# Performance work log

Measured on AMD Instinct MI355X. Metric: run time of the kernel, lower is better.

## Reference

```python
import jax, jax.numpy as jnp
import numpy as np

E, D, H, F = 1024, 64, 16, 4096  # embedding, per-head dim, heads, mlp hidden
B, S = 2, 2048
EPS = 1e-5


def _layernorm(x, g, b):
    m = jnp.mean(x, axis=-1, keepdims=True)
    v = jnp.mean((x - m) ** 2, axis=-1, keepdims=True)
    return (x - m) * jax.lax.rsqrt(v + EPS) * g + b


def setup_inputs() -> dict:
    key = jax.random.key(0)
    ks = jax.random.split(key, 12)
    s_e = 1.0 / np.sqrt(E)
    s_f = 1.0 / np.sqrt(F)
    return {
        "x": jax.random.normal(ks[0], (B, S, E), jnp.float32),
        "Wq": jax.random.normal(ks[1], (H, E, D), jnp.float32) * s_e,
        "bq": jnp.zeros((H, D), jnp.float32),
        "Wk": jax.random.normal(ks[2], (H, E, D), jnp.float32) * s_e,
        "bk": jnp.zeros((H, D), jnp.float32),
        "Wv": jax.random.normal(ks[3], (H, E, D), jnp.float32) * s_e,
        "bv": jnp.zeros((H, D), jnp.float32),
        "Wo": jax.random.normal(ks[4], (E, E), jnp.float32) * s_e,
        "bo": jnp.zeros((E,), jnp.float32),
        "ln1_g": jnp.ones((E,), jnp.float32),
        "ln1_b": jnp.zeros((E,), jnp.float32),
        "ln2_g": jnp.ones((E,), jnp.float32),
        "ln2_b": jnp.zeros((E,), jnp.float32),
        "W1": jax.random.normal(ks[5], (E, F), jnp.float32) * s_e,
        "b1": jnp.zeros((F,), jnp.float32),
        "W2": jax.random.normal(ks[6], (F, E), jnp.float32) * s_f,
        "b2": jnp.zeros((E,), jnp.float32),
    }


def reference(x, Wq, bq, Wk, bk, Wv, bv, Wo, bo, ln1_g, ln1_b, ln2_g, ln2_b, W1, b1, W2, b2):
    h = _layernorm(x, ln1_g, ln1_b)
    # batched-head projections: [H,B,S,D]
    q = jnp.einsum("bse,hed->hbsd", h, Wq) + bq[:, None, None, :]
    k = jnp.einsum("bse,hed->hbsd", h, Wk) + bk[:, None, None, :]
    v = jnp.einsum("bse,hed->hbsd", h, Wv) + bv[:, None, None, :]
    # faithful quirk: scores = K @ Q^T (no 1/sqrt(d)), softmax over query axis
    scores = jnp.einsum("hbsd,hbtd->hbst", k, q)  # [H,B,S_key,S_query]
    att = jax.nn.softmax(scores, axis=-1)
    o = jnp.einsum("hbst,hbtd->hbsd", att, v)  # [H,B,S,D]
    o = jnp.transpose(o, (1, 2, 0, 3)).reshape(x.shape[0], x.shape[1], -1)  # concat heads
    x = x + o @ Wo + bo
    m = _layernorm(x, ln2_g, ln2_b)
    m = jax.nn.relu(m @ W1 + b1) @ W2 + b2
    return x + m
```

## Files before the change

### kernel.cpp

```cpp
#include <hip/hip_runtime.h>
#include <cstdint>
#include <cstddef>

typedef __attribute__((ext_vector_type(8))) short short8;
typedef __attribute__((ext_vector_type(4))) float f32x4;
typedef __attribute__((ext_vector_type(4))) unsigned short ushort4v;

#define E_DIM 1024
#define D_DIM 64
#define H_DIM 16
#define F_DIM 4096
#define B_DIM 2
#define S_DIM 2048
#define M_DIM 4096
#define LN_EPS 1e-5f

__device__ __forceinline__ float bf2f(unsigned short u) {
  union { unsigned int i; float f; } v;
  v.i = ((unsigned int)u) << 16;
  return v.f;
}
__device__ __forceinline__ unsigned short f2bf(float f) {
  union { float f; unsigned int i; } v;
  v.f = f;
  unsigned int r = v.i + 0x7FFFu + ((v.i >> 16) & 1u);
  return (unsigned short)(r >> 16);
}

__device__ __forceinline__ void gload_lds16(const unsigned short* src,
                                            unsigned short* dst) {
  __builtin_amdgcn_global_load_lds(
      (const __attribute__((address_space(1))) void*)src,
      (__attribute__((address_space(3))) void*)dst, 16, 0, 0);
}

template <bool QKV>
__global__ __launch_bounds__(256) void transpose_w(
    const float* __restrict__ in, unsigned short* __restrict__ ohi, int R,
    int C) {
  __shared__ float t[32][33];
  const int c0 = blockIdx.x * 32, r0 = blockIdx.y * 32;
  const int tid = threadIdx.x;
  {
    const int rr = tid >> 3, c4 = (tid & 7) * 4;
    size_t addr;
    if (QKV)
      addr = (size_t)(c0 >> 6) * 65536 + (size_t)(r0 + rr) * 64 +
             ((c0 & 63) + c4);
    else
      addr = (size_t)(r0 + rr) * C + (c0 + c4);
    float4 v = *(const float4*)(in + addr);
    t[rr][c4 + 0] = v.x;
    t[rr][c4 + 1] = v.y;
    t[rr][c4 + 2] = v.z;
    t[rr][c4 + 3] = v.w;
  }
  __syncthreads();
  {
    const int cc = tid >> 3, k4 = (tid & 7) * 4;
    ushort4v hi;
    hi.x = f2bf(t[k4 + 0][cc]);
    hi.y = f2bf(t[k4 + 1][cc]);
    hi.z = f2bf(t[k4 + 2][cc]);
    hi.w = f2bf(t[k4 + 3][cc]);
    *(ushort4v*)(ohi + (size_t)(c0 + cc) * R + (r0 + k4)) = hi;
  }
}

__global__ __launch_bounds__(256) void ln_kernel(const float* __restrict__ x,
                                                 const float* __restrict__ g,
                                                 const float* __restrict__ b,
                                                 unsigned short* __restrict__ o) {
  const int row = blockIdx.x;
  const float* xp = x + (size_t)row * E_DIM;
  const int t4 = threadIdx.x * 4;
  float4 xv = *(const float4*)(xp + t4);
  float s = xv.x + xv.y + xv.z + xv.w;
  float ss = xv.x * xv.x + xv.y * xv.y + xv.z * xv.z + xv.w * xv.w;
#pragma unroll
  for (int off = 32; off > 0; off >>= 1) {
    s += __shfl_down(s, off);
    ss += __shfl_down(ss, off);
  }
  __shared__ float red[8];
  const int wid = threadIdx.x >> 6;
  if ((threadIdx.x & 63) == 0) {
    red[wid] = s;
    red[4 + wid] = ss;
  }
  __syncthreads();
  if (threadIdx.x == 0) {
    float S = red[0] + red[1] + red[2] + red[3];
    float SS = red[4] + red[5] + red[6] + red[7];
    float mean = S * (1.0f / E_DIM);
    float var = SS * (1.0f / E_DIM) - mean * mean;
    red[0] = mean;
    red[1] = rsqrtf(var + LN_EPS);
  }
  __syncthreads();
  const float mean = red[0], rstd = red[1];
  float4 gv = *(const float4*)(g + t4);
  float4 bv = *(const float4*)(b + t4);
  ushort4v hi;
  hi.x = f2bf((xv.x - mean) * rstd * gv.x + bv.x);
  hi.y = f2bf((xv.y - mean) * rstd * gv.y + bv.y);
  hi.z = f2bf((xv.z - mean) * rstd * gv.z + bv.z);
  hi.w = f2bf((xv.w - mean) * rstd * gv.w + bv.w);
  *(ushort4v*)(o + (size_t)row * E_DIM + t4) = hi;
}

template <int MODE>
__global__ __launch_bounds__(256) void mfma_gemm(
    const unsigned short* __restrict__ A, const unsigned short* __restrict__ B,
    const float* __restrict__ bias, const float* __restrict__ bias2,
    const float* __restrict__ bias3, const float* __restrict__ resid,
    void* __restrict__ out0, void* __restrict__ out1, void* __restrict__ out2,
    int M, int N, int K) {
  __shared__ unsigned short As[8192];
  __shared__ unsigned short Bs[8192];
  const int tid = threadIdx.x;
  const int m0 = blockIdx.y * 128, n0 = blockIdx.x * 128;
  const int lane = tid & 63, wid = tid >> 6;
  const int wr = wid >> 1, wc = wid & 1;
  const int lr = lane & 15, lg = lane >> 4;

  f32x4 acc[4][4];
#pragma unroll
  for (int i = 0; i < 4; ++i)
#pragma unroll
    for (int j = 0; j < 4; ++j) acc[i][j] = {0.f, 0.f, 0.f, 0.f};

  const int kbeg = (MODE == 4) ? blockIdx.z * 1024 : 0;
  const int kend = (MODE == 4) ? kbeg + 1024 : K;

  for (int k0 = kbeg; k0 < kend; k0 += 64) {
#pragma unroll
    for (int c = 0; c < 4; ++c) {
      int slot = tid + 256 * c;
      int r = slot >> 3;
      int cb = ((slot & 7) << 4) ^ ((r & 7) << 4);
      int ldsoff = tid * 8 + c * 2048;
      gload_lds16(A + (size_t)(m0 + r) * K + k0 + (cb >> 1), As + ldsoff);
      gload_lds16(B + (size_t)(n0 + r) * K + k0 + (cb >> 1), Bs + ldsoff);
    }
    __syncthreads();
#pragma unroll
    for (int kc = 0; kc < 2; ++kc) {
      short8 af[4], bf[4];
#pragma unroll
      for (int mi = 0; mi < 4; ++mi) {
        int r = wr * 64 + mi * 16 + lr;
        int cb = (kc * 64 + lg * 16) ^ ((r & 7) << 4);
        af[mi] = *(const short8*)(As + r * 64 + (cb >> 1));
      }
#pragma unroll
      for (int ni = 0; ni < 4; ++ni) {
        int r = wc * 64 + ni * 16 + lr;
        int cb = (kc * 64 + lg * 16) ^ ((r & 7) << 4);
        bf[ni] = *(const short8*)(Bs + r * 64 + (cb >> 1));
      }
#pragma unroll
      for (int mi = 0; mi < 4; ++mi)
#pragma unroll
        for (int ni = 0; ni < 4; ++ni)
          acc[mi][ni] = __builtin_amdgcn_mfma_f32_16x16x32_bf16(
              af[mi], bf[ni], acc[mi][ni], 0, 0, 0);
    }
    __syncthreads();
  }
#pragma unroll
  for (int mi = 0; mi < 4; ++mi) {
#pragma unroll
    for (int ni = 0; ni < 4; ++ni) {
      int n = n0 + wc * 64 + ni * 16 + lr;
#pragma unroll
      for (int rr = 0; rr < 4; ++rr) {
        int m = m0 + wr * 64 + mi * 16 + lg * 4 + rr;
        float v = acc[mi][ni][rr];
        if constexpr (MODE == 0) {
          int seg = n >> 10, nn = n & 1023;
          const float* bp = seg == 0 ? bias : seg == 1 ? bias2 : bias3;
          v += bp[nn];
          int hh = nn >> 6, d = nn & 63, bb = m >> 11, srow = m & 2047;
          size_t pb = (size_t)(hh * 2 + bb) * 131072;
          if (seg == 0)
            ((unsigned short*)out0)[pb + (size_t)srow * 64 + d] = f2bf(v);
          else if (seg == 1)
            ((unsigned short*)out1)[pb + (size_t)srow * 64 + d] = f2bf(v);
          else
            ((unsigned short*)out2)[pb + (size_t)d * 2048 + srow] = f2bf(v);
        } else if constexpr (MODE == 2) {
          size_t ad = (size_t)m * N + n;
          ((float*)out0)[ad] = v + bias[n] + resid[ad];
        } else if constexpr (MODE == 3) {
          ((unsigned short*)out0)[(size_t)m * N + n] = f2bf(fmaxf(v + bias[n], 0.f));
        } else {
          unsafeAtomicAdd((float*)out0 + (size_t)m * N + n, v);
        }
      }
    }
  }
}

__global__ __launch_bounds__(256, 4) void attn_mfma(
    const unsigned short* __restrict__ Q, const unsigned short* __restrict__ K,
    const unsigned short* __restrict__ Vt, unsigned short* __restrict__ O) {
  __shared__ unsigned short Qs[2][4096];
  __shared__ unsigned short Vs[2][4096];
  const int bid = blockIdx.x;
  const int wg = (bid & 7) * 128 + (bid >> 3);
  const int pair = wg >> 5, stile = wg & 31;
  const int tid = threadIdx.x, lane = tid & 63, wid = tid >> 6;
  const int lr = lane & 15, lg = lane >> 4;
  const size_t pbase = (size_t)pair * 131072;

  const int s_own = stile * 64 + wid * 16 + lr;
  short8 kb[2];
#pragma unroll
  for (int c = 0; c < 2; ++c)
    kb[c] = *(const short8*)(K + pbase + (size_t)s_own * 64 + c * 32 + lg * 8);

  f32x4 oa[4];
#pragma unroll
  for (int i = 0; i < 4; ++i) oa[i] = {0.f, 0.f, 0.f, 0.f};
  float mrun = -3e38f, lrun = 0.f;

  auto stage = [&](int buf, int t0) {
#pragma unroll
    for (int c = 0; c < 2; ++c) {
      int slot = tid + 256 * c;
      int r = slot >> 3;
      int cb = ((slot & 7) << 4) ^ ((r & 7) << 4);
      gload_lds16(Q + pbase + (size_t)(t0 + r) * 64 + (cb >> 1),
                  &Qs[buf][slot * 8]);
      gload_lds16(Vt + pbase + (size_t)r * 2048 + t0 + (cb >> 1),
                  &Vs[buf][slot * 8]);
    }
  };

  stage(0, 0);
  __syncthreads();

  for (int it = 0; it < 32; ++it) {
    const int cur = it & 1;
    if (it < 31) stage(cur ^ 1, (it + 1) * 64);

    f32x4 sacc[4];
#pragma unroll
    for (int j = 0; j < 4; ++j) {
      sacc[j] = {0.f, 0.f, 0.f, 0.f};
#pragma unroll
      for (int c = 0; c < 2; ++c) {
        int row = j * 16 + lr;
        int cb = (c * 64 + lg * 16) ^ ((row & 7) << 4);
        short8 aq = *(const short8*)(&Qs[cur][row * 64 + (cb >> 1)]);
        sacc[j] = __builtin_amdgcn_mfma_f32_16x16x32_bf16(aq, kb[c], sacc[j], 0, 0, 0);
      }
    }
    float mj0 = fmaxf(fmaxf(sacc[0][0], sacc[0][1]), fmaxf(sacc[0][2], sacc[0][3]));
    float mj1 = fmaxf(fmaxf(sacc[1][0], sacc[1][1]), fmaxf(sacc[1][2], sacc[1][3]));
    float mj2 = fmaxf(fmaxf(sacc[2][0], sacc[2][1]), fmaxf(sacc[2][2], sacc[2][3]));
    float mj3 = fmaxf(fmaxf(sacc[3][0], sacc[3][1]), fmaxf(sacc[3][2], sacc[3][3]));
    float tm = fmaxf(fmaxf(mj0, mj1), fmaxf(mj2, mj3));
    tm = fmaxf(tm, __shfl_xor(tm, 16));
    tm = fmaxf(tm, __shfl_xor(tm, 32));
    float mnew = fmaxf(mrun, tm);
    float scale = __expf(mrun - mnew);
    mrun = mnew;
    float p[4][4];
#pragma unroll
    for (int j = 0; j < 4; ++j)
#pragma unroll
      for (int r = 0; r < 4; ++r) p[j][r] = __expf(sacc[j][r] - mnew);
    float lsum = ((p[0][0] + p[0][1]) + (p[0][2] + p[0][3])) +
                 ((p[1][0] + p[1][1]) + (p[1][2] + p[1][3])) +
                 ((p[2][0] + p[2][1]) + (p[2][2] + p[2][3])) +
                 ((p[3][0] + p[3][1]) + (p[3][2] + p[3][3]));
    lsum += __shfl_xor(lsum, 16);
    lsum += __shfl_xor(lsum, 32);
    lrun = lrun * scale + lsum;
#pragma unroll
    for (int di = 0; di < 4; ++di) {
      f32x4 t = oa[di];
      t[0] *= scale; t[1] *= scale; t[2] *= scale; t[3] *= scale;
      oa[di] = t;
    }
    unsigned int pw[4][2];
#pragma unroll
    for (int j = 0; j < 4; ++j) {
      pw[j][0] = (unsigned)f2bf(p[j][0]) | ((unsigned)f2bf(p[j][1]) << 16);
      pw[j][1] = (unsigned)f2bf(p[j][2]) | ((unsigned)f2bf(p[j][3]) << 16);
    }
#pragma unroll
    for (int kc = 0; kc < 2; ++kc) {
      unsigned int bw[4];
#pragma unroll
      for (int mm = 0; mm < 4; ++mm) {
        int src = ((lg & 1) * 2 + (mm >> 1)) * 16 + lr;
        int lo = __shfl((int)pw[2 * kc][mm & 1], src, 64);
        int hi = __shfl((int)pw[2 * kc + 1][mm & 1], src, 64);
        bw[mm] = (lg & 2) ? (unsigned)hi : (unsigned)lo;
      }
      union { unsigned int u[4]; short8 s8; } pb;
      pb.u[0] = bw[0]; pb.u[1] = bw[1]; pb.u[2] = bw[2]; pb.u[3] = bw[3];
#pragma unroll
      for (int di = 0; di < 4; ++di) {
        int row = di * 16 + lr;
        int cb = (kc * 64 + lg * 16) ^ ((row & 7) << 4);
        short8 vf = *(const short8*)(&Vs[cur][row * 64 + (cb >> 1)]);
        oa[di] = __builtin_amdgcn_mfma_f32_16x16x32_bf16(vf, pb.s8, oa[di], 0, 0, 0);
      }
    }
    __syncthreads();
  }

  const float inv = 1.f / lrun;
  const int b = pair & 1, h = pair >> 1;
  unsigned short* op = O + ((size_t)(b * 2048 + s_own)) * 1024 + h * 64;
#pragma unroll
  for (int di = 0; di < 4; ++di) {
    unsigned int w0 = (unsigned)f2bf(oa[di][0] * inv) |
                      ((unsigned)f2bf(oa[di][1] * inv) << 16);
    unsigned int w1 = (unsigned)f2bf(oa[di][2] * inv) |
                      ((unsigned)f2bf(oa[di][3] * inv) << 16);
    *(unsigned int*)(op + di * 16 + lg * 4) = w0;
    *(unsigned int*)(op + di * 16 + lg * 4 + 2) = w1;
  }
}

__global__ __launch_bounds__(256) void init_out(const float* __restrict__ x2,
                                                const float* __restrict__ b2,
                                                float* __restrict__ out) {
  int i = blockIdx.x * 256 + threadIdx.x;
  float4 v = ((const float4*)x2)[i];
  float4 bb = ((const float4*)b2)[i & 255];
  v.x += bb.x; v.y += bb.y; v.z += bb.z; v.w += bb.w;
  ((float4*)out)[i] = v;
}

extern "C" void kernel_launch(void* const* d_in, const int* in_sizes, int n_in,
                              void* d_out, int out_size, void* d_ws,
                              size_t ws_size, hipStream_t stream) {
  const float* x = (const float*)d_in[0];
  const float* Wq = (const float*)d_in[1];
  const float* bq = (const float*)d_in[2];
  const float* Wk = (const float*)d_in[3];
  const float* bk = (const float*)d_in[4];
  const float* Wv = (const float*)d_in[5];
  const float* bv = (const float*)d_in[6];
  const float* Wo = (const float*)d_in[7];
  const float* bo = (const float*)d_in[8];
  const float* ln1_g = (const float*)d_in[9];
  const float* ln1_b = (const float*)d_in[10];
  const float* ln2_g = (const float*)d_in[11];
  const float* ln2_b = (const float*)d_in[12];
  const float* W1 = (const float*)d_in[13];
  const float* b1 = (const float*)d_in[14];
  const float* W2 = (const float*)d_in[15];
  const float* b2 = (const float*)d_in[16];

  char* w = (char*)d_ws;
  const size_t MB = 1024 * 1024;
  unsigned short* WqkvT = (unsigned short*)(w + 0 * MB);
  unsigned short* WoT = (unsigned short*)(w + 6 * MB);
  unsigned short* W1T = (unsigned short*)(w + 8 * MB);
  unsigned short* W2T = (unsigned short*)(w + 16 * MB);
  unsigned short* h = (unsigned short*)(w + 24 * MB);
  unsigned short* Qb = (unsigned short*)(w + 32 * MB);
  unsigned short* Kb = (unsigned short*)(w + 40 * MB);
  unsigned short* Vt = (unsigned short*)(w + 48 * MB);
  unsigned short* Obuf = (unsigned short*)(w + 56 * MB);
  unsigned short* m1 = (unsigned short*)(w + 32 * MB);
  float* x2 = (float*)(w + 64 * MB);

  const dim3 blk(256);

  transpose_w<true><<<dim3(32, 32), blk, 0, stream>>>(Wq, WqkvT, 1024, 1024);
  transpose_w<true><<<dim3(32, 32), blk, 0, stream>>>(Wk, WqkvT + 1048576, 1024, 1024);
  transpose_w<true><<<dim3(32, 32), blk, 0, stream>>>(Wv, WqkvT + 2097152, 1024, 1024);
  transpose_w<false><<<dim3(32, 32), blk, 0, stream>>>(Wo, WoT, 1024, 1024);
  transpose_w<false><<<dim3(128, 32), blk, 0, stream>>>(W1, W1T, 1024, 4096);
  transpose_w<false><<<dim3(32, 128), blk, 0, stream>>>(W2, W2T, 4096, 1024);

  ln_kernel<<<M_DIM, blk, 0, stream>>>(x, ln1_g, ln1_b, h);

  mfma_gemm<0><<<dim3(24, 32), blk, 0, stream>>>(h, WqkvT, bq, bk, bv, nullptr,
                                                 Qb, Kb, Vt, M_DIM, 3072, 1024);

  attn_mfma<<<1024, blk, 0, stream>>>(Qb, Kb, Vt, Obuf);

  mfma_gemm<2><<<dim3(8, 32), blk, 0, stream>>>(Obuf, WoT, bo, nullptr, nullptr,
                                                x, x2, nullptr, nullptr, M_DIM,
                                                1024, 1024);

  ln_kernel<<<M_DIM, blk, 0, stream>>>(x2, ln2_g, ln2_b, h);

  mfma_gemm<3><<<dim3(32, 32), blk, 0, stream>>>(h, W1T, b1, nullptr, nullptr,
                                                 nullptr, m1, nullptr, nullptr,
                                                 M_DIM, 4096, 1024);

  init_out<<<4096, blk, 0, stream>>>(x2, b2, (float*)d_out);

  mfma_gemm<4><<<dim3(8, 32, 4), blk, 0, stream>>>(
      m1, W2T, nullptr, nullptr, nullptr, nullptr, (float*)d_out, nullptr,
      nullptr, M_DIM, 1024, 4096);
}
```

Baseline: 421.3 us.

## Use fragment-ordered LDS layout, exp2 softmax with lazy rescale, split-K out-proj

Shared-memory tiles in the GEMM and attention kernels are now stored in MFMA fragment order, so each lane reads a contiguous 16-byte chunk and the XOR swizzle arithmetic is gone. Q weights and bias are pre-scaled by log2(e), so the softmax uses the raw v_exp_f32 instruction and only rescales the running max and accumulators when the max grows past a threshold. Packed bf16 conversion instructions and s_setprio around MFMA blocks are added. The output projection becomes split-K with atomics into a pre-initialised residual-plus-bias buffer, and the W2 GEMM split drops from 4 to 2. The lazy rescale adds a small numerical risk, and the atomics add contention and an extra init pass.

```diff
diff --git a/kernel.cpp b/kernel.cpp
--- a/kernel.cpp
+++ b/kernel.cpp
@@ -14,6 +14,7 @@
 #define S_DIM 2048
 #define M_DIM 4096
 #define LN_EPS 1e-5f
+#define LOG2E 1.4426950408889634f
 
 __device__ __forceinline__ float bf2f(unsigned short u) {
   union { unsigned int i; float f; } v;
@@ -26,6 +27,16 @@
   unsigned int r = v.i + 0x7FFFu + ((v.i >> 16) & 1u);
   return (unsigned short)(r >> 16);
 }
+__device__ __forceinline__ unsigned int cvt_pk_bf16(float a, float b) {
+  unsigned int r;
+  asm("v_cvt_pk_bf16_f32 %0, %1, %2" : "=v"(r) : "v"(a), "v"(b));
+  return r;
+}
+__device__ __forceinline__ float exp2_fast(float x) {
+  float r;
+  asm("v_exp_f32 %0, %1" : "=v"(r) : "v"(x));
+  return r;
+}
 
 __device__ __forceinline__ void gload_lds16(const unsigned short* src,
                                             unsigned short* dst) {
@@ -37,7 +48,7 @@
 template <bool QKV>
 __global__ __launch_bounds__(256) void transpose_w(
     const float* __restrict__ in, unsigned short* __restrict__ ohi, int R,
-    int C) {
+    int C, float scale) {
   __shared__ float t[32][33];
   const int c0 = blockIdx.x * 32, r0 = blockIdx.y * 32;
   const int tid = threadIdx.x;
@@ -59,10 +70,10 @@
   {
     const int cc = tid >> 3, k4 = (tid & 7) * 4;
     ushort4v hi;
-    hi.x = f2bf(t[k4 + 0][cc]);
-    hi.y = f2bf(t[k4 + 1][cc]);
-    hi.z = f2bf(t[k4 + 2][cc]);
-    hi.w = f2bf(t[k4 + 3][cc]);
+    hi.x = f2bf(t[k4 + 0][cc] * scale);
+    hi.y = f2bf(t[k4 + 1][cc] * scale);
+    hi.z = f2bf(t[k4 + 2][cc] * scale);
+    hi.w = f2bf(t[k4 + 3][cc] * scale);
     *(ushort4v*)(ohi + (size_t)(c0 + cc) * R + (r0 + k4)) = hi;
   }
 }
@@ -113,9 +124,8 @@
 __global__ __launch_bounds__(256) void mfma_gemm(
     const unsigned short* __restrict__ A, const unsigned short* __restrict__ B,
     const float* __restrict__ bias, const float* __restrict__ bias2,
-    const float* __restrict__ bias3, const float* __restrict__ resid,
-    void* __restrict__ out0, void* __restrict__ out1, void* __restrict__ out2,
-    int M, int N, int K) {
+    const float* __restrict__ bias3, void* __restrict__ out0,
+    void* __restrict__ out1, void* __restrict__ out2, int M, int N, int K) {
   __shared__ unsigned short As[8192];
   __shared__ unsigned short Bs[8192];
   const int tid = threadIdx.x;
@@ -130,41 +140,40 @@
 #pragma unroll
     for (int j = 0; j < 4; ++j) acc[i][j] = {0.f, 0.f, 0.f, 0.f};
 
-  const int kbeg = (MODE == 4) ? blockIdx.z * 1024 : 0;
-  const int kend = (MODE == 4) ? kbeg + 1024 : K;
+  int kbeg = 0, kend = K;
+  if constexpr (MODE == 4) {
+    int kslice = K / gridDim.z;
+    kbeg = blockIdx.z * kslice;
+    kend = kbeg + kslice;
+  }
 
   for (int k0 = kbeg; k0 < kend; k0 += 64) {
 #pragma unroll
     for (int c = 0; c < 4; ++c) {
-      int slot = tid + 256 * c;
-      int r = slot >> 3;
-      int cb = ((slot & 7) << 4) ^ ((r & 7) << 4);
-      int ldsoff = tid * 8 + c * 2048;
-      gload_lds16(A + (size_t)(m0 + r) * K + k0 + (cb >> 1), As + ldsoff);
-      gload_lds16(B + (size_t)(n0 + r) * K + k0 + (cb >> 1), Bs + ldsoff);
+      int chunk = wid * 4 + c;
+      int rb = chunk >> 1, kc = chunk & 1;
+      size_t goff = (size_t)(rb * 16 + lr) * K + k0 + kc * 32 + lg * 8;
+      gload_lds16(A + (size_t)m0 * K + goff, As + chunk * 512);
+      gload_lds16(B + (size_t)n0 * K + goff, Bs + chunk * 512);
     }
     __syncthreads();
 #pragma unroll
     for (int kc = 0; kc < 2; ++kc) {
       short8 af[4], bf[4];
 #pragma unroll
-      for (int mi = 0; mi < 4; ++mi) {
-        int r = wr * 64 + mi * 16 + lr;
-        int cb = (kc * 64 + lg * 16) ^ ((r & 7) << 4);
-        af[mi] = *(const short8*)(As + r * 64 + (cb >> 1));
-      }
-#pragma unroll
-      for (int ni = 0; ni < 4; ++ni) {
-        int r = wc * 64 + ni * 16 + lr;
-        int cb = (kc * 64 + lg * 16) ^ ((r & 7) << 4);
-        bf[ni] = *(const short8*)(Bs + r * 64 + (cb >> 1));
-      }
+      for (int mi = 0; mi < 4; ++mi)
+        af[mi] = *(const short8*)(As + ((wr * 4 + mi) * 2 + kc) * 512 + lane * 8);
+#pragma unroll
+      for (int ni = 0; ni < 4; ++ni)
+        bf[ni] = *(const short8*)(Bs + ((wc * 4 + ni) * 2 + kc) * 512 + lane * 8);
+      __builtin_amdgcn_s_setprio(1);
 #pragma unroll
       for (int mi = 0; mi < 4; ++mi)
 #pragma unroll
         for (int ni = 0; ni < 4; ++ni)
           acc[mi][ni] = __builtin_amdgcn_mfma_f32_16x16x32_bf16(
               af[mi], bf[ni], acc[mi][ni], 0, 0, 0);
+      __builtin_amdgcn_s_setprio(0);
     }
     __syncthreads();
   }
@@ -180,7 +189,7 @@
         if constexpr (MODE == 0) {
           int seg = n >> 10, nn = n & 1023;
           const float* bp = seg == 0 ? bias : seg == 1 ? bias2 : bias3;
-          v += bp[nn];
+          v += (seg == 0) ? bp[nn] * LOG2E : bp[nn];
           int hh = nn >> 6, d = nn & 63, bb = m >> 11, srow = m & 2047;
           size_t pb = (size_t)(hh * 2 + bb) * 131072;
           if (seg == 0)
@@ -189,9 +198,6 @@
             ((unsigned short*)out1)[pb + (size_t)srow * 64 + d] = f2bf(v);
           else
             ((unsigned short*)out2)[pb + (size_t)d * 2048 + srow] = f2bf(v);
-        } else if constexpr (MODE == 2) {
-          size_t ad = (size_t)m * N + n;
-          ((float*)out0)[ad] = v + bias[n] + resid[ad];
         } else if constexpr (MODE == 3) {
           ((unsigned short*)out0)[(size_t)m * N + n] = f2bf(fmaxf(v + bias[n], 0.f));
         } else {
@@ -228,13 +234,11 @@
   auto stage = [&](int buf, int t0) {
 #pragma unroll
     for (int c = 0; c < 2; ++c) {
-      int slot = tid + 256 * c;
-      int r = slot >> 3;
-      int cb = ((slot & 7) << 4) ^ ((r & 7) << 4);
-      gload_lds16(Q + pbase + (size_t)(t0 + r) * 64 + (cb >> 1),
-                  &Qs[buf][slot * 8]);
-      gload_lds16(Vt + pbase + (size_t)r * 2048 + t0 + (cb >> 1),
-                  &Vs[buf][slot * 8]);
+      int chunk = wid * 2 + c;
+      gload_lds16(Q + pbase + (size_t)(t0 + wid * 16 + lr) * 64 + c * 32 + lg * 8,
+                  &Qs[buf][chunk * 512]);
+      gload_lds16(Vt + pbase + (size_t)(wid * 16 + lr) * 2048 + t0 + c * 32 + lg * 8,
+                  &Vs[buf][chunk * 512]);
     }
   };
 
@@ -249,47 +253,50 @@
 #pragma unroll
     for (int j = 0; j < 4; ++j) {
       sacc[j] = {0.f, 0.f, 0.f, 0.f};
+      __builtin_amdgcn_s_setprio(1);
 #pragma unroll
       for (int c = 0; c < 2; ++c) {
-        int row = j * 16 + lr;
-        int cb = (c * 64 + lg * 16) ^ ((row & 7) << 4);
-        short8 aq = *(const short8*)(&Qs[cur][row * 64 + (cb >> 1)]);
+        short8 aq = *(const short8*)(&Qs[cur][(j * 2 + c) * 512 + lane * 8]);
         sacc[j] = __builtin_amdgcn_mfma_f32_16x16x32_bf16(aq, kb[c], sacc[j], 0, 0, 0);
       }
-    }
-    float mj0 = fmaxf(fmaxf(sacc[0][0], sacc[0][1]), fmaxf(sacc[0][2], sacc[0][3]));
-    float mj1 = fmaxf(fmaxf(sacc[1][0], sacc[1][1]), fmaxf(sacc[1][2], sacc[1][3]));
-    float mj2 = fmaxf(fmaxf(sacc[2][0], sacc[2][1]), fmaxf(sacc[2][2], sacc[2][3]));
-    float mj3 = fmaxf(fmaxf(sacc[3][0], sacc[3][1]), fmaxf(sacc[3][2], sacc[3][3]));
-    float tm = fmaxf(fmaxf(mj0, mj1), fmaxf(mj2, mj3));
+      __builtin_amdgcn_s_setprio(0);
+    }
+    float tm = fmaxf(
+        fmaxf(fmaxf(fmaxf(sacc[0][0], sacc[0][1]), fmaxf(sacc[0][2], sacc[0][3])),
+              fmaxf(fmaxf(sacc[1][0], sacc[1][1]), fmaxf(sacc[1][2], sacc[1][3]))),
+        fmaxf(fmaxf(fmaxf(sacc[2][0], sacc[2][1]), fmaxf(sacc[2][2], sacc[2][3])),
+              fmaxf(fmaxf(sacc[3][0], sacc[3][1]), fmaxf(sacc[3][2], sacc[3][3]))));
     tm = fmaxf(tm, __shfl_xor(tm, 16));
     tm = fmaxf(tm, __shfl_xor(tm, 32));
-    float mnew = fmaxf(mrun, tm);
-    float scale = __expf(mrun - mnew);
-    mrun = mnew;
+    if (!__all(tm - mrun <= 11.0f)) {
+      float mnew = fmaxf(mrun, tm);
+      float sc = exp2_fast(mrun - mnew);
+      mrun = mnew;
+      lrun *= sc;
+#pragma unroll
+      for (int di = 0; di < 4; ++di) {
+        f32x4 t = oa[di];
+        t[0] *= sc; t[1] *= sc; t[2] *= sc; t[3] *= sc;
+        oa[di] = t;
+      }
+    }
     float p[4][4];
 #pragma unroll
     for (int j = 0; j < 4; ++j)
 #pragma unroll
-      for (int r = 0; r < 4; ++r) p[j][r] = __expf(sacc[j][r] - mnew);
+      for (int r = 0; r < 4; ++r) p[j][r] = exp2_fast(sacc[j][r] - mrun);
     float lsum = ((p[0][0] + p[0][1]) + (p[0][2] + p[0][3])) +
                  ((p[1][0] + p[1][1]) + (p[1][2] + p[1][3])) +
                  ((p[2][0] + p[2][1]) + (p[2][2] + p[2][3])) +
                  ((p[3][0] + p[3][1]) + (p[3][2] + p[3][3]));
     lsum += __shfl_xor(lsum, 16);
     lsum += __shfl_xor(lsum, 32);
-    lrun = lrun * scale + lsum;
-#pragma unroll
-    for (int di = 0; di < 4; ++di) {
-      f32x4 t = oa[di];
-      t[0] *= scale; t[1] *= scale; t[2] *= scale; t[3] *= scale;
-      oa[di] = t;
-    }
+    lrun += lsum;
     unsigned int pw[4][2];
 #pragma unroll
     for (int j = 0; j < 4; ++j) {
-      pw[j][0] = (unsigned)f2bf(p[j][0]) | ((unsigned)f2bf(p[j][1]) << 16);
-      pw[j][1] = (unsigned)f2bf(p[j][2]) | ((unsigned)f2bf(p[j][3]) << 16);
+      pw[j][0] = cvt_pk_bf16(p[j][0], p[j][1]);
+      pw[j][1] = cvt_pk_bf16(p[j][2], p[j][3]);
     }
 #pragma unroll
     for (int kc = 0; kc < 2; ++kc) {
@@ -303,13 +310,13 @@
       }
       union { unsigned int u[4]; short8 s8; } pb;
       pb.u[0] = bw[0]; pb.u[1] = bw[1]; pb.u[2] = bw[2]; pb.u[3] = bw[3];
+      __builtin_amdgcn_s_setprio(1);
 #pragma unroll
       for (int di = 0; di < 4; ++di) {
-        int row = di * 16 + lr;
-        int cb = (kc * 64 + lg * 16) ^ ((row & 7) << 4);
-        short8 vf = *(const short8*)(&Vs[cur][row * 64 + (cb >> 1)]);
+        short8 vf = *(const short8*)(&Vs[cur][(di * 2 + kc) * 512 + lane * 8]);
         oa[di] = __builtin_amdgcn_mfma_f32_16x16x32_bf16(vf, pb.s8, oa[di], 0, 0, 0);
       }
+      __builtin_amdgcn_s_setprio(0);
     }
     __syncthreads();
   }
@@ -319,21 +326,19 @@
   unsigned short* op = O + ((size_t)(b * 2048 + s_own)) * 1024 + h * 64;
 #pragma unroll
   for (int di = 0; di < 4; ++di) {
-    unsigned int w0 = (unsigned)f2bf(oa[di][0] * inv) |
-                      ((unsigned)f2bf(oa[di][1] * inv) << 16);
-    unsigned int w1 = (unsigned)f2bf(oa[di][2] * inv) |
-                      ((unsigned)f2bf(oa[di][3] * inv) << 16);
+    unsigned int w0 = cvt_pk_bf16(oa[di][0] * inv, oa[di][1] * inv);
+    unsigned int w1 = cvt_pk_bf16(oa[di][2] * inv, oa[di][3] * inv);
     *(unsigned int*)(op + di * 16 + lg * 4) = w0;
     *(unsigned int*)(op + di * 16 + lg * 4 + 2) = w1;
   }
 }
 
-__global__ __launch_bounds__(256) void init_out(const float* __restrict__ x2,
-                                                const float* __restrict__ b2,
+__global__ __launch_bounds__(256) void init_acc(const float* __restrict__ resid,
+                                                const float* __restrict__ bias,
                                                 float* __restrict__ out) {
   int i = blockIdx.x * 256 + threadIdx.x;
-  float4 v = ((const float4*)x2)[i];
-  float4 bb = ((const float4*)b2)[i & 255];
+  float4 v = ((const float4*)resid)[i];
+  float4 bb = ((const float4*)bias)[i & 255];
   v.x += bb.x; v.y += bb.y; v.z += bb.z; v.w += bb.w;
   ((float4*)out)[i] = v;
 }
@@ -375,33 +380,33 @@
 
   const dim3 blk(256);
 
-  transpose_w<true><<<dim3(32, 32), blk, 0, stream>>>(Wq, WqkvT, 1024, 1024);
-  transpose_w<true><<<dim3(32, 32), blk, 0, stream>>>(Wk, WqkvT + 1048576, 1024, 1024);
-  transpose_w<true><<<dim3(32, 32), blk, 0, stream>>>(Wv, WqkvT + 2097152, 1024, 1024);
-  transpose_w<false><<<dim3(32, 32), blk, 0, stream>>>(Wo, WoT, 1024, 1024);
-  transpose_w<false><<<dim3(128, 32), blk, 0, stream>>>(W1, W1T, 1024, 4096);
-  transpose_w<false><<<dim3(32, 128), blk, 0, stream>>>(W2, W2T, 4096, 1024);
+  transpose_w<true><<<dim3(32, 32), blk, 0, stream>>>(Wq, WqkvT, 1024, 1024, LOG2E);
+  transpose_w<true><<<dim3(32, 32), blk, 0, stream>>>(Wk, WqkvT + 1048576, 1024, 1024, 1.f);
+  transpose_w<true><<<dim3(32, 32), blk, 0, stream>>>(Wv, WqkvT + 2097152, 1024, 1024, 1.f);
+  transpose_w<false><<<dim3(32, 32), blk, 0, stream>>>(Wo, WoT, 1024, 1024, 1.f);
+  transpose_w<false><<<dim3(128, 32), blk, 0, stream>>>(W1, W1T, 1024, 4096, 1.f);
+  transpose_w<false><<<dim3(32, 128), blk, 0, stream>>>(W2, W2T, 4096, 1024, 1.f);
 
   ln_kernel<<<M_DIM, blk, 0, stream>>>(x, ln1_g, ln1_b, h);
 
-  mfma_gemm<0><<<dim3(24, 32), blk, 0, stream>>>(h, WqkvT, bq, bk, bv, nullptr,
-                                                 Qb, Kb, Vt, M_DIM, 3072, 1024);
+  mfma_gemm<0><<<dim3(24, 32), blk, 0, stream>>>(h, WqkvT, bq, bk, bv, Qb, Kb,
+                                                 Vt, M_DIM, 3072, 1024);
 
   attn_mfma<<<1024, blk, 0, stream>>>(Qb, Kb, Vt, Obuf);
 
-  mfma_gemm<2><<<dim3(8, 32), blk, 0, stream>>>(Obuf, WoT, bo, nullptr, nullptr,
-                                                x, x2, nullptr, nullptr, M_DIM,
-                                                1024, 1024);
+  init_acc<<<4096, blk, 0, stream>>>(x, bo, x2);
+  mfma_gemm<4><<<dim3(8, 32, 2), blk, 0, stream>>>(Obuf, WoT, nullptr, nullptr,
+                                                   nullptr, x2, nullptr,
+                                                   nullptr, M_DIM, 1024, 1024);
 
   ln_kernel<<<M_DIM, blk, 0, stream>>>(x2, ln2_g, ln2_b, h);
 
   mfma_gemm<3><<<dim3(32, 32), blk, 0, stream>>>(h, W1T, b1, nullptr, nullptr,
-                                                 nullptr, m1, nullptr, nullptr,
-                                                 M_DIM, 4096, 1024);
-
-  init_out<<<4096, blk, 0, stream>>>(x2, b2, (float*)d_out);
-
-  mfma_gemm<4><<<dim3(8, 32, 4), blk, 0, stream>>>(
-      m1, W2T, nullptr, nullptr, nullptr, nullptr, (float*)d_out, nullptr,
-      nullptr, M_DIM, 1024, 4096);
-}
+                                                 m1, nullptr, nullptr, M_DIM,
+                                                 4096, 1024);
+
+  init_acc<<<4096, blk, 0, stream>>>(x2, b2, (float*)d_out);
+  mfma_gemm<4><<<dim3(8, 32, 2), blk, 0, stream>>>(
+      m1, W2T, nullptr, nullptr, nullptr, (float*)d_out, nullptr, nullptr,
+      M_DIM, 1024, 4096);
+}
```

After: 494.2 us. 17.3% more time.
